# Kernel tuning notes

Measured on AMD Instinct MI355X. Metric: run time of the kernel, lower is better.

Reference implementation:

```python
import jax, jax.numpy as jnp
import numpy as np

NR_TRIALS = 5000
KERNEL_LEN = 201
KERNEL_STD = 30.0

# Gaussian smoothing window: signal.gaussian(201, std=30) with first 100 taps zeroed (causal half)
def _make_window():
    w = np.exp(-0.5 * ((np.arange(KERNEL_LEN) - 100) / KERNEL_STD) ** 2)
    w[:100] = 0.0
    return jnp.asarray(w, dtype=jnp.float32)

WINDOW = _make_window()


def setup_inputs() -> dict:
    key = jax.random.key(0)
    ks = jax.random.split(key, 10)
    B, N, T, H, S = 512, 8192, NR_TRIALS, 5, 10
    max_val = float(np.sqrt(1.0 / H))
    inp = {
        "x": jax.random.normal(ks[0], (B, N), dtype=jnp.float32),
        "history": jax.random.normal(ks[1], (B, N, H), dtype=jnp.float32),
        "gain": jax.random.normal(ks[2], (B,), dtype=jnp.float32),  # unused, kept for signature parity
        "state": jax.random.normal(ks[3], (B, S), dtype=jnp.float32),
        "sort_id": jax.random.randint(ks[4], (B, 1), 0, T, dtype=jnp.int64),
        "history_weights": jax.random.uniform(ks[5], (N, H), minval=-max_val, maxval=max_val, dtype=jnp.float32),
        "history_bias": jax.random.uniform(ks[6], (N,), minval=-max_val, maxval=max_val, dtype=jnp.float32),
        "state_W": jax.random.normal(ks[7], (N, S), dtype=jnp.float32) * 0.3,  # nn.Linear(S -> N) weight
        "state_b": jax.random.normal(ks[8], (N,), dtype=jnp.float32) * 0.1,
        "own_gain": jax.random.normal(ks[9], (T,), dtype=jnp.float32) * 0.1,
        "gain_adjust": jnp.ones((N,), dtype=jnp.float32),
    }
    return inp


def reference(x, history, gain, state, sort_id, history_weights, history_bias,
              state_W, state_b, own_gain, gain_adjust):
    # history modulation: einsum over the small history dim + bias
    hist = jnp.einsum("bnh,nh->bn", history, history_weights) + history_bias
    x = x + hist
    # behavioral state encoder (Linear S->N) + elu, added to x
    state_mod = state @ state_W.T + state_b
    x = x + jax.nn.elu(state_mod)
    x = jax.nn.elu(x) + 1.0
    # gain path: conv1d('same', 201-tap kernel) of a one-hot at sort_id, dotted with own_gain,
    # is exactly a windowed gather-dot: batch_gain[b] = sum_k WINDOW[k] * own_gain[sort_id[b] + 100 - k]
    T = own_gain.shape[0]
    s = sort_id[:, 0].astype(jnp.int32)                      # [B]
    idx = s[:, None] + 100 - jnp.arange(KERNEL_LEN)          # [B, 201]
    valid = (idx >= 0) & (idx < T)
    g = jnp.where(valid, own_gain[jnp.clip(idx, 0, T - 1)], 0.0)
    batch_gain = (g * WINDOW).sum(axis=-1, keepdims=True)    # [B, 1] (channel dim e=1)
    batch_gain = jax.nn.elu(batch_gain) + 1.0
    # per-neuron gain adjust
    x = (1.0 + gain_adjust[None, :] * batch_gain) * x
    return x
```

## Files before the change

kernel.cpp:

```cpp
#include <hip/hip_runtime.h>
#include <math.h>
#include <stdint.h>

#define Bsz 512
#define Nn 8192
#define Hh 5
#define Ss 10
#define KB 4
#define TILE 1024
#define NT 256
#define TILES (Nn / TILE)
#define REG (TILE * Hh)

__device__ __forceinline__ float elu1(float v) {
    return v > 0.0f ? v : expm1f(v);
}

__device__ __forceinline__ void stage_region(const float* __restrict__ g,
                                             float* l, int wave, int lane) {
    #pragma unroll
    for (int p = 0; p < 5; ++p) {
        int off = wave * 1280 + p * 256;
        __builtin_amdgcn_global_load_lds(
            (const __attribute__((address_space(1))) uint32_t*)(g + off + lane * 4),
            (__attribute__((address_space(3))) uint32_t*)(l + off),
            16, 0, 0);
    }
}

__global__ __launch_bounds__(NT, 4) void main_kernel(
    const float* __restrict__ x,
    const float* __restrict__ history,
    const float* __restrict__ state,
    const float* __restrict__ hw,
    const float* __restrict__ hb,
    const float* __restrict__ sW,
    const float* __restrict__ sb,
    const float* __restrict__ ga,
    const int*   __restrict__ sort_id,
    const float* __restrict__ own_gain,
    float* __restrict__ out)
{
    __shared__ __align__(16) float lds[2 * REG];

    const int tid  = threadIdx.x;
    const int lane = tid & 63;
    const int wave = tid >> 6;
    const int tile  = blockIdx.x & (TILES - 1);
    const int chunk = blockIdx.x / TILES;
    const int n0 = tile * TILE;
    const int b0 = chunk * KB;
    const int nq = n0 + tid * 4;

    float bgv[KB];
    {
        int grp = lane >> 4;
        int r   = lane & 15;
        int s   = sort_id[b0 + grp];
        int jmax = s < 100 ? s : 100;
        float acc = 0.0f;
        #pragma unroll
        for (int k = 0; k < 7; ++k) {
            int j = r + k * 16;
            if (j <= jmax) {
                float t = (float)j * (1.0f / 30.0f);
                acc = fmaf(expf(-0.5f * t * t), own_gain[s - j], acc);
            }
        }
        acc += __shfl_xor(acc, 1);
        acc += __shfl_xor(acc, 2);
        acc += __shfl_xor(acc, 4);
        acc += __shfl_xor(acc, 8);
        #pragma unroll
        for (int g = 0; g < KB; ++g)
            bgv[g] = elu1(__shfl(acc, g * 16)) + 1.0f;
    }

    float4 hbv = *reinterpret_cast<const float4*>(hb + nq);
    float4 sbv = *reinterpret_cast<const float4*>(sb + nq);
    float4 gav = *reinterpret_cast<const float4*>(ga + nq);

    stage_region(hw + (size_t)n0 * Hh, lds, wave, lane);
    __syncthreads();
    float wA[20];
    #pragma unroll
    for (int i = 0; i < 5; ++i) {
        float4 t = *reinterpret_cast<float4*>(&lds[tid * 20 + i * 4]);
        wA[i*4+0] = t.x; wA[i*4+1] = t.y; wA[i*4+2] = t.z; wA[i*4+3] = t.w;
    }
    __syncthreads();

    stage_region(sW + (size_t)n0 * Ss,       lds,       wave, lane);
    stage_region(sW + (size_t)n0 * Ss + REG, lds + REG, wave, lane);
    __syncthreads();
    float wS[40];
    #pragma unroll
    for (int i = 0; i < 10; ++i) {
        float4 t = *reinterpret_cast<float4*>(&lds[tid * 40 + i * 4]);
        wS[i*4+0] = t.x; wS[i*4+1] = t.y; wS[i*4+2] = t.z; wS[i*4+3] = t.w;
    }
    __syncthreads();

    stage_region(history + ((size_t)b0 * Nn + n0) * Hh, lds, wave, lane);
    __syncthreads();

    #pragma unroll
    for (int kb = 0; kb < KB; ++kb) {
        const int b = b0 + kb;
        float* buf = lds + (kb & 1) * REG;

        if (kb + 1 < KB)
            stage_region(history + ((size_t)(b + 1) * Nn + n0) * Hh,
                         lds + ((kb + 1) & 1) * REG, wave, lane);

        float st[Ss];
        #pragma unroll
        for (int i = 0; i < Ss; ++i) st[i] = state[b * Ss + i];

        float4 xv = *reinterpret_cast<const float4*>(x + (size_t)b * Nn + nq);

        float hist[4] = {hbv.x, hbv.y, hbv.z, hbv.w};
        #pragma unroll
        for (int i = 0; i < 5; ++i) {
            float4 h = *reinterpret_cast<float4*>(&buf[tid * 20 + i * 4]);
            float hv4[4] = {h.x, h.y, h.z, h.w};
            #pragma unroll
            for (int j = 0; j < 4; ++j) {
                int f = i * 4 + j;
                hist[f / Hh] = fmaf(hv4[j], wA[f], hist[f / Hh]);
            }
        }

        float sm[4] = {sbv.x, sbv.y, sbv.z, sbv.w};
        #pragma unroll
        for (int f = 0; f < 40; ++f)
            sm[f / Ss] = fmaf(st[f % Ss], wS[f], sm[f / Ss]);

        float xa[4]  = {xv.x, xv.y, xv.z, xv.w};
        float gaa[4] = {gav.x, gav.y, gav.z, gav.w};
        float res[4];
        #pragma unroll
        for (int q = 0; q < 4; ++q) {
            float v = xa[q] + hist[q] + elu1(sm[q]);
            res[q] = fmaf(gaa[q], bgv[kb], 1.0f) * (elu1(v) + 1.0f);
        }
        *reinterpret_cast<float4*>(out + (size_t)b * Nn + nq) =
            make_float4(res[0], res[1], res[2], res[3]);

        __syncthreads();
    }
}

extern "C" void kernel_launch(void* const* d_in, const int* in_sizes, int n_in,
                              void* d_out, int out_size, void* d_ws, size_t ws_size,
                              hipStream_t stream) {
    const float* x        = (const float*)d_in[0];
    const float* history  = (const float*)d_in[1];
    const float* state    = (const float*)d_in[3];
    const int*   sort_id  = (const int*)d_in[4];
    const float* hw       = (const float*)d_in[5];
    const float* hb       = (const float*)d_in[6];
    const float* sW       = (const float*)d_in[7];
    const float* sb       = (const float*)d_in[8];
    const float* own_gain = (const float*)d_in[9];
    const float* ga       = (const float*)d_in[10];
    float* out = (float*)d_out;

    const int nblocks = TILES * (Bsz / KB);
    main_kernel<<<nblocks, NT, 0, stream>>>(x, history, state, hw, hb, sW, sb,
                                            ga, sort_id, own_gain, out);
}
```

Before: 27.84 us.

## Use per-wave LDS regions to drop block barriers and double KB

```diff
diff --git a/kernel.cpp b/kernel.cpp
--- a/kernel.cpp
+++ b/kernel.cpp
@@ -6,29 +6,24 @@
 #define Nn 8192
 #define Hh 5
 #define Ss 10
-#define KB 4
+#define KB 8
 #define TILE 1024
 #define NT 256
 #define TILES (Nn / TILE)
-#define REG (TILE * Hh)
+
+#define LDS_FLOATS 15360
 
 __device__ __forceinline__ float elu1(float v) {
     return v > 0.0f ? v : expm1f(v);
 }
 
-__device__ __forceinline__ void stage_region(const float* __restrict__ g,
-                                             float* l, int wave, int lane) {
-    #pragma unroll
-    for (int p = 0; p < 5; ++p) {
-        int off = wave * 1280 + p * 256;
-        __builtin_amdgcn_global_load_lds(
-            (const __attribute__((address_space(1))) uint32_t*)(g + off + lane * 4),
-            (__attribute__((address_space(3))) uint32_t*)(l + off),
-            16, 0, 0);
-    }
+__device__ __forceinline__ void gload16(const float* src, float* dst) {
+    __builtin_amdgcn_global_load_lds(
+        (const __attribute__((address_space(1))) uint32_t*)src,
+        (__attribute__((address_space(3))) uint32_t*)dst, 16, 0, 0);
 }
 
-__global__ __launch_bounds__(NT, 4) void main_kernel(
+__global__ __launch_bounds__(NT, 2) void main_kernel(
     const float* __restrict__ x,
     const float* __restrict__ history,
     const float* __restrict__ state,
@@ -41,7 +36,7 @@
     const float* __restrict__ own_gain,
     float* __restrict__ out)
 {
-    __shared__ __align__(16) float lds[2 * REG];
+    __shared__ __align__(16) float lds[LDS_FLOATS];
 
     const int tid  = threadIdx.x;
     const int lane = tid & 63;
@@ -52,16 +47,23 @@
     const int b0 = chunk * KB;
     const int nq = n0 + tid * 4;
 
+    float* myreg = &lds[wave * 2560];
+    float* myhw  = &lds[10240 + wave * 1280];
+
+    float4 hbv = *reinterpret_cast<const float4*>(hb + nq);
+    float4 sbv = *reinterpret_cast<const float4*>(sb + nq);
+    float4 gav = *reinterpret_cast<const float4*>(ga + nq);
+
     float bgv[KB];
     {
-        int grp = lane >> 4;
-        int r   = lane & 15;
+        int grp = lane >> 3;
+        int r   = lane & 7;
         int s   = sort_id[b0 + grp];
         int jmax = s < 100 ? s : 100;
         float acc = 0.0f;
         #pragma unroll
-        for (int k = 0; k < 7; ++k) {
-            int j = r + k * 16;
+        for (int k = 0; k < 13; ++k) {
+            int j = r + k * 8;
             if (j <= jmax) {
                 float t = (float)j * (1.0f / 30.0f);
                 acc = fmaf(expf(-0.5f * t * t), own_gain[s - j], acc);
@@ -70,59 +72,66 @@
         acc += __shfl_xor(acc, 1);
         acc += __shfl_xor(acc, 2);
         acc += __shfl_xor(acc, 4);
-        acc += __shfl_xor(acc, 8);
         #pragma unroll
         for (int g = 0; g < KB; ++g)
-            bgv[g] = elu1(__shfl(acc, g * 16)) + 1.0f;
+            bgv[g] = elu1(__shfl(acc, g * 8)) + 1.0f;
     }
 
-    float4 hbv = *reinterpret_cast<const float4*>(hb + nq);
-    float4 sbv = *reinterpret_cast<const float4*>(sb + nq);
-    float4 gav = *reinterpret_cast<const float4*>(ga + nq);
+    {
+        const float* srcS = sW + (size_t)n0 * Ss + wave * 2560 + lane * 4;
+        #pragma unroll
+        for (int p = 0; p < 10; ++p) gload16(srcS + p * 256, myreg + p * 256);
+        const float* srcA = hw + (size_t)n0 * Hh + wave * 1280 + lane * 4;
+        #pragma unroll
+        for (int p = 0; p < 5; ++p)  gload16(srcA + p * 256, myhw + p * 256);
+    }
+    asm volatile("s_waitcnt vmcnt(0)" ::: "memory");
 
-    stage_region(hw + (size_t)n0 * Hh, lds, wave, lane);
-    __syncthreads();
-    float wA[20];
+    float wS[40], wA[20];
+    #pragma unroll
+    for (int i = 0; i < 10; ++i) {
+        float4 t = *reinterpret_cast<float4*>(&myreg[lane * 40 + i * 4]);
+        wS[i*4+0] = t.x; wS[i*4+1] = t.y; wS[i*4+2] = t.z; wS[i*4+3] = t.w;
+    }
     #pragma unroll
     for (int i = 0; i < 5; ++i) {
-        float4 t = *reinterpret_cast<float4*>(&lds[tid * 20 + i * 4]);
+        float4 t = *reinterpret_cast<float4*>(&myhw[lane * 20 + i * 4]);
         wA[i*4+0] = t.x; wA[i*4+1] = t.y; wA[i*4+2] = t.z; wA[i*4+3] = t.w;
     }
-    __syncthreads();
+    asm volatile("" ::: "memory");
 
-    stage_region(sW + (size_t)n0 * Ss,       lds,       wave, lane);
-    stage_region(sW + (size_t)n0 * Ss + REG, lds + REG, wave, lane);
-    __syncthreads();
-    float wS[40];
-    #pragma unroll
-    for (int i = 0; i < 10; ++i) {
-        float4 t = *reinterpret_cast<float4*>(&lds[tid * 40 + i * 4]);
-        wS[i*4+0] = t.x; wS[i*4+1] = t.y; wS[i*4+2] = t.z; wS[i*4+3] = t.w;
+    {
+        const float* src = history + ((size_t)b0 * Nn + n0) * Hh + wave * 1280 + lane * 4;
+        #pragma unroll
+        for (int p = 0; p < 5; ++p) gload16(src + p * 256, myreg + p * 256);
     }
-    __syncthreads();
-
-    stage_region(history + ((size_t)b0 * Nn + n0) * Hh, lds, wave, lane);
-    __syncthreads();
+    float4 xv = *reinterpret_cast<const float4*>(x + (size_t)b0 * Nn + nq);
 
     #pragma unroll
     for (int kb = 0; kb < KB; ++kb) {
         const int b = b0 + kb;
-        float* buf = lds + (kb & 1) * REG;
 
-        if (kb + 1 < KB)
-            stage_region(history + ((size_t)(b + 1) * Nn + n0) * Hh,
-                         lds + ((kb + 1) & 1) * REG, wave, lane);
+        asm volatile("s_waitcnt vmcnt(0)" ::: "memory");
+
+        float4 xnext = xv;
+        if (kb + 1 < KB) {
+            const float* src = history + ((size_t)(b + 1) * Nn + n0) * Hh
+                               + wave * 1280 + lane * 4;
+            float* dst = myreg + ((kb + 1) & 1) * 1280;
+            #pragma unroll
+            for (int p = 0; p < 5; ++p) gload16(src + p * 256, dst + p * 256);
+            xnext = *reinterpret_cast<const float4*>(x + (size_t)(b + 1) * Nn + nq);
+        }
 
         float st[Ss];
         #pragma unroll
         for (int i = 0; i < Ss; ++i) st[i] = state[b * Ss + i];
 
-        float4 xv = *reinterpret_cast<const float4*>(x + (size_t)b * Nn + nq);
-
+        const float* buf = myreg + (kb & 1) * 1280 + lane * 20;
         float hist[4] = {hbv.x, hbv.y, hbv.z, hbv.w};
         #pragma unroll
         for (int i = 0; i < 5; ++i) {
-            float4 h = *reinterpret_cast<float4*>(&buf[tid * 20 + i * 4]);
+            float4 h = *reinterpret_cast<const float4*>(buf + i * 4);
             float hv4[4] = {h.x, h.y, h.z, h.w};
             #pragma unroll
             for (int j = 0; j < 4; ++j) {
@@ -147,7 +156,7 @@
         *reinterpret_cast<float4*>(out + (size_t)b * Nn + nq) =
             make_float4(res[0], res[1], res[2], res[3]);
 
-        __syncthreads();
+        xv = xnext;
     }
 }
 
```

Result: faster. 27.13 us, median of 4 (-2.5%).
